# Performance work log

Hardware: AMD Instinct MI355X
Metric: run time of the kernel (lower is better)

## Reference

```python
import jax, jax.numpy as jnp
import numpy as np

K_DT = 7
GAMMA_DT = 0.1
EPS = 1e-6
B_DIST = 3.0

def _make_kernels():
    # CDT kernel: exp(-dist/gamma), 7x7x7
    k = K_DT
    g = np.mgrid[0:k, 0:k, 0:k] - np.floor(k / 2)
    dist = np.sqrt((g ** 2).sum(axis=0))
    cdt_k = np.exp(-dist / GAMMA_DT)[None, None].astype(np.float32)  # [1,1,7,7,7]
    # 27-point Laplacian
    lap = (1.0 / 26.0) * np.array(
        [[[2, 3, 2], [3, 6, 3], [2, 3, 2]],
         [[3, 6, 3], [6, -88, 6], [3, 6, 3]],
         [[2, 3, 2], [3, 6, 3], [2, 3, 2]]], dtype=np.float64)
    lap_k = lap[None, None].astype(np.float32)  # [1,1,3,3,3]
    # Scharr_2 Sobel-type gradient filters
    h1_p = np.array([[[1, 0, -1]]], dtype=np.float64)
    h1 = np.array([[[47, 162, 47]]], dtype=np.float64)
    h1 = h1 / h1.sum()
    h2 = h1.transpose(1, 2, 0); h2_p = h1_p.transpose(1, 2, 0)
    h3 = h1.transpose(2, 0, 1); h3_p = h1_p.transpose(2, 0, 1)
    G1 = np.kron(np.kron(h2, h3), h1_p)
    G2 = np.kron(np.kron(h3, h1), h2_p)
    G3 = np.kron(np.kron(h1, h2), h3_p)
    sob_k = np.stack([G1, G2, G3], axis=0)[:, None].astype(np.float32)  # [3,1,3,3,3]
    return jnp.asarray(cdt_k), jnp.asarray(lap_k), jnp.asarray(sob_k)

CDT_K, LAP_K, SOB_K = _make_kernels()

def conv3d(x, w, pad):
    return jax.lax.conv_general_dilated(
        x, w, window_strides=(1, 1, 1), padding=[(pad, pad)] * 3,
        dimension_numbers=('NCDHW', 'OIDHW', 'NCDHW'))

def binary(x, th, gamma):
    return jax.nn.sigmoid((x - th) * gamma)

def cdt(x):
    return -GAMMA_DT * jnp.log(conv3d(x, CDT_K, 3) + EPS)

def setup_inputs() -> dict:
    key = jax.random.key(0)
    k1, k2, k3 = jax.random.split(key, 3)
    B, C, D, H, W = 2, 1, 128, 192, 192
    x_in = jax.random.uniform(k1, (B, C, D, H, W), dtype=jnp.float32)
    y_out = jax.random.normal(k2, (B, C, D, H, W), dtype=jnp.float32)
    y_tg = jax.random.randint(k3, (B, C, D, H, W), 0, 2).astype(jnp.float32)
    w_smp = jnp.ones((1,), dtype=jnp.float32)
    gamma_ace = jnp.full((1,), 0.1, dtype=jnp.float32)
    return {"x_in": x_in, "y_out": y_out, "y_tg": y_tg, "w_smp": w_smp, "gamma_ace": gamma_ace}

def reference(x_in, y_out, y_tg, w_smp, gamma_ace):
    w_mean = jnp.mean(w_smp)
    # ---- CE_Loss (BCEWithLogits, pos_weight=1, stable form) ----
    ce_pt = jnp.clip(y_out, 0, None) - y_out * y_tg + jnp.log1p(jnp.exp(-jnp.abs(y_out)))
    ce_pm = jnp.mean(ce_pt, axis=(1, 2, 3))  # matches torch mean over dims (1,2,3)
    loss_ce = jnp.mean(w_smp * ce_pm) / w_mean
    # ---- Dice_Loss ----
    y_p = jax.nn.sigmoid(y_out)
    inter = jnp.sum(y_p * y_tg, axis=(1, 2, 3))
    card = jnp.sum(y_p + y_tg, axis=(1, 2, 3))
    d_loss = 1.0 - 2.0 * inter / (card + EPS)
    loss_dice = jnp.mean(w_smp * d_loss) / w_mean
    # ---- DT_Loss ----
    y_p_inv = 1.0 - y_p
    yb = binary(y_p, 0.5, 200.0)
    yb_inv = binary(y_p_inv, 0.5, 200.0)
    y_tg_inv = 1.0 - y_tg
    z = cdt(yb); z_tg = cdt(y_tg); z_inv = cdt(yb_inv); z_tg_inv = cdt(y_tg_inv)
    dl1 = jnp.mean(y_tg * z) / jnp.mean(y_tg + EPS)
    dl2 = jnp.mean(y_p * z_tg) / jnp.mean(y_p + EPS)
    dl3 = jnp.mean(y_tg_inv * z_inv) / jnp.mean(y_tg_inv + EPS)
    dl4 = jnp.mean(y_p_inv * z_tg_inv) / jnp.mean(y_p_inv + EPS)
    dt_pt = dl1 + dl2 + dl3 + dl4
    loss_dt = jnp.mean(w_smp * dt_pt) / w_mean
    # ---- ACE_Loss ----
    y = binary(y_p, 0.5, 200.0)
    y1 = binary(conv3d(y, LAP_K, 1), 0.5, 200.0)        # edge detector
    s = conv3d(y, SOB_K, 1)                              # [B,3,D,H,W]
    y2 = jnp.sqrt(jnp.sum(s * s, axis=1, keepdims=True) + EPS)
    y3 = jax.nn.relu(B_DIST - cdt(y))
    y4 = binary((B_DIST - y3) * binary(y3, 0.0, 200.0), 0.1, 200.0)
    l1 = jnp.mean(x_in * y, axis=(1, 2, 3, 4)) / jnp.mean(y + EPS, axis=(1, 2, 3, 4))
    l2 = jnp.mean(x_in * y4, axis=(1, 2, 3, 4)) / jnp.mean(y4 + EPS, axis=(1, 2, 3, 4))
    E1 = jnp.mean(y * (x_in - l1[:, None, None, None, None]) ** 2) / jnp.mean(y + EPS)
    E2 = jnp.mean(y4 * (x_in - l2[:, None, None, None, None]) ** 2) / jnp.mean(y4 + EPS)
    S = jnp.mean(y1 * y2) / jnp.mean(y1 + EPS)
    ace_pt = E1 + E2 + gamma_ace[0] * S
    loss_ace = jnp.mean(w_smp * ace_pt) / w_mean
    # ---- weighted sum ----
    w_ce, w_dt, w_ace, w_dice = 1.0, 0.1, 0.1, 1.0
    return w_ce * loss_ce + w_dice * loss_dice + w_dt * loss_dt + w_ace * loss_ace
```

## Files before the change

### kernel.cpp

```cpp
#include <hip/hip_runtime.h>
#include <hip/hip_bf16.h>

#define TH 8
#define TW 64
#define DC 16
#define PH (TH+2)
#define PW (TW+2)
#define PN (PH*PW)

#define DIM_D 128
#define DIM_H 192
#define DIM_W 192
#define NREP 16

#define LOG2E 1.4426950408889634f
#define LN2   0.6931471805599453f

__device__ __forceinline__ float ex2(float x){ return __builtin_amdgcn_exp2f(x); }
__device__ __forceinline__ float lg2(float x){ return __builtin_amdgcn_logf(x); }
__device__ __forceinline__ float rcpf_(float x){ return __builtin_amdgcn_rcpf(x); }
__device__ __forceinline__ float2 f2add(float2 a, float2 b){ return make_float2(a.x+b.x, a.y+b.y); }
__device__ __forceinline__ float2 f2fma(float s, float2 a, float2 b){
    return make_float2(fmaf(s,a.x,b.x), fmaf(s,a.y,b.y));
}

struct Pair { float2 u0[2], u1[2], u2[2]; float s1[2], s2[2]; };

__device__ __forceinline__ Pair calc_pair(const float2* __restrict__ sp, int ty, int tx)
{
    const float S30 = 47.f/256.f, S31 = 162.f/256.f;
    float2 c[3][4];
    #pragma unroll
    for (int r = 0; r < 3; ++r) {
        const float2* row = sp + (ty+r)*PW + 2*tx;
        float4 lo = *reinterpret_cast<const float4*>(row);
        float4 hi = *reinterpret_cast<const float4*>(row + 2);
        c[r][0] = make_float2(lo.x, lo.y); c[r][1] = make_float2(lo.z, lo.w);
        c[r][2] = make_float2(hi.x, hi.y); c[r][3] = make_float2(hi.z, hi.w);
    }
    float2 s[4], m[4]; float dj[4];
    #pragma unroll
    for (int j = 0; j < 4; ++j) {
        s[j] = f2add(c[0][j], c[2][j]);
        m[j] = c[1][j];
        dj[j] = c[0][j].x - c[2][j].x;
    }
    Pair P;
    float2 mm02 = f2add(m[0], m[2]), mm13 = f2add(m[1], m[3]);
    P.u0[0] = m[1];              P.u0[1] = m[2];
    P.u1[0] = f2add(s[1], mm02); P.u1[1] = f2add(s[2], mm13);
    P.u2[0] = f2add(s[0], s[2]); P.u2[1] = f2add(s[1], s[3]);
    P.s1[0] = S30*(s[0].x - s[2].x) + S31*(m[0].x - m[2].x);
    P.s1[1] = S30*(s[1].x - s[3].x) + S31*(m[1].x - m[3].x);
    P.s2[0] = S30*(dj[0] + dj[2]) + S31*dj[1];
    P.s2[1] = S30*(dj[1] + dj[3]) + S31*dj[2];
    return P;
}

__global__ __launch_bounds__(256) void lumen_main(
    const float* __restrict__ x_in, const float* __restrict__ y_out,
    const float* __restrict__ y_tg, double* __restrict__ gacc,
    float* __restrict__ dice_i, float* __restrict__ dice_c)
{
    __shared__ float2 ring[4][PN];

    const int tid = threadIdx.x;
    const int b  = blockIdx.z >> 3;
    const int d0 = (blockIdx.z & 7) * DC;
    const int h0 = blockIdx.y * TH;
    const int w0 = blockIdx.x * TW;
    const unsigned base = (unsigned)b * (unsigned)(DIM_D*DIM_H*DIM_W);
    const unsigned PL = DIM_H*DIM_W;
    const int rep = (blockIdx.x + gridDim.x*(blockIdx.y + gridDim.y*blockIdx.z)) & (NREP-1);

    const int l1v = tid + 256, l2v = tid + 512;
    const int dy0 = tid / PW, dx0 = tid - dy0*PW;
    const int dy1 = l1v / PW, dx1 = l1v - dy1*PW;
    const int dy2 = l2v / PW, dx2 = l2v - dy2*PW;
    const bool w2  = (l2v < PN);
    const int sgh0 = h0-1+dy0, sgw0 = w0-1+dx0;
    const int sgh1 = h0-1+dy1, sgw1 = w0-1+dx1;
    const int sgh2 = h0-1+dy2, sgw2 = w0-1+dx2;
    const bool ok0 = ((unsigned)sgh0 < (unsigned)DIM_H) && ((unsigned)sgw0 < (unsigned)DIM_W);
    const bool ok1 = ((unsigned)sgh1 < (unsigned)DIM_H) && ((unsigned)sgw1 < (unsigned)DIM_W);
    const bool ok2 = w2 && ((unsigned)sgh2 < (unsigned)DIM_H) && ((unsigned)sgw2 < (unsigned)DIM_W);
    const unsigned soff0 = ok0 ? (unsigned)(sgh0*DIM_W + sgw0) : 0u;
    const unsigned soff1 = ok1 ? (unsigned)(sgh1*DIM_W + sgw1) : 0u;
    const unsigned soff2 = ok2 ? (unsigned)(sgh2*DIM_W + sgw2) : 0u;

    float ld_yo0, ld_tg0, ld_yo1, ld_tg1, ld_yo2, ld_tg2;

    auto LOADP = [&](int p){
        if ((unsigned)p < (unsigned)DIM_D) {
            const unsigned pb = base + (unsigned)p*PL;
            float a0 = y_out[pb + soff0], c0 = y_tg[pb + soff0];
            float a1_ = y_out[pb + soff1], c1 = y_tg[pb + soff1];
            float a2_ = y_out[pb + soff2], c2 = y_tg[pb + soff2];
            ld_yo0 = ok0 ? a0 : -1e30f;  ld_tg0 = ok0 ? c0 : 0.f;
            ld_yo1 = ok1 ? a1_ : -1e30f; ld_tg1 = ok1 ? c1 : 0.f;
            ld_yo2 = ok2 ? a2_ : -1e30f; ld_tg2 = ok2 ? c2 : 0.f;
        } else {
            ld_yo0 = -1e30f; ld_tg0 = 0.f; ld_yo1 = -1e30f; ld_tg1 = 0.f;
            ld_yo2 = -1e30f; ld_tg2 = 0.f;
        }
    };
    auto WRITEP = [&](int slot){
        float yb0 = rcpf_(1.f + ex2(-50.f*LOG2E*ld_yo0));
        ring[slot][tid] = make_float2(yb0, ld_tg0);
        float yb1 = rcpf_(1.f + ex2(-50.f*LOG2E*ld_yo1));
        ring[slot][l1v] = make_float2(yb1, ld_tg1);
        if (w2) {
            float yb2 = rcpf_(1.f + ex2(-50.f*LOG2E*ld_yo2));
            ring[slot][l2v] = make_float2(yb2, ld_tg2);
        }
    };

    const int ty = tid >> 5, tx = tid & 31;
    const int gh = h0 + ty;
    const float2* xin2 = reinterpret_cast<const float2*>(x_in);
    const float2* yo2p = reinterpret_cast<const float2*>(y_out);
    const unsigned PL2 = PL >> 1;
    const unsigned cen2 = (base >> 1) + (unsigned)gh*(DIM_W/2) + (unsigned)(w0>>1) + (unsigned)tx;

    const float KC1 = 4.5399929762484854e-05f, KC2 = 7.2135410e-07f, KC3 = 3.0047e-08f;
    const float L0 = -88.f/26.f, L1 = 6.f/26.f, L2 = 3.f/26.f, L3 = 2.f/26.f;
    const float S30 = 47.f/256.f, S31 = 162.f/256.f;
    const float TFULL = 1.f + 6.f*KC1 + 12.f*KC2 + 8.f*KC3;
    const float Y4TH = 0.36787858f;

    LOADP(d0-1); WRITEP(3);
    LOADP(d0  ); WRITEP(0);
    LOADP(d0+1); WRITEP(1);
    LOADP(d0+2);
    __syncthreads();
    Pair PA = calc_pair(ring[3], ty, tx);
    Pair PB = calc_pair(ring[0], ty, tx);

    float a_ce=0, a_tz=0, a_pzt=0, a_itzi=0, a_ipzti=0, a_ytg=0;
    float a_y1y2=0, a_y1=0;
    float2 aE1 = make_float2(0.f,0.f);
    float2 aEx = make_float2(0.f,0.f);
    float2 aExx= make_float2(0.f,0.f);
    float dI0=0, dI1=0, dC0=0, dC1=0;

    #pragma unroll 2
    for (int i = 0; i < DC; ++i) {
        const int d = d0 + i;
        WRITEP((i+2)&3);
        __syncthreads();
        LOADP(d+3);
        float2 xc  = xin2[cen2 + (unsigned)d*PL2];
        float2 yoc = yo2p[cen2 + (unsigned)d*PL2];

        Pair PC = calc_pair(ring[(i+1)&3], ty, tx);

        #pragma unroll
        for (int v = 0; v < 2; ++v) {
            float2 q0 = f2add(PA.u0[v], PC.u0[v]);
            float2 q1 = f2add(PA.u1[v], PC.u1[v]);
            float2 q2 = f2add(PA.u2[v], PC.u2[v]);
            float2 acv = f2fma(KC3, q2,
                         f2fma(KC2, f2add(PB.u2[v], q1),
                         f2fma(KC1, f2add(PB.u1[v], q0), PB.u0[v])));
            float acx = acv.x, act = acv.y;
            float al  = L0*PB.u0[v].x + L1*(PB.u1[v].x + q0.x)
                      + L2*(PB.u2[v].x + q1.x) + L3*q2.x;
            float a1 = S30*(PA.s1[v] + PC.s1[v]) + S31*PB.s1[v];
            float a2 = S30*(PA.s2[v] + PC.s2[v]) + S31*PB.s2[v];
            float a3 = (S31*S31)*(PA.u0[v].x - PC.u0[v].x)
                     + (S30*S31)*(PA.u1[v].x - PC.u1[v].x)
                     + (S30*S30)*(PA.u2[v].x - PC.u2[v].x);

            float t   = PB.u0[v].y;
            float ybc = PB.u0[v].x;
            float x   = v ? xc.y  : xc.x;
            float yo  = v ? yoc.y : yoc.x;

            float ayo = fabsf(yo);
            float e1  = ex2(-LOG2E*ayo);
            float inv = rcpf_(1.f + e1);
            float yp  = (yo >= 0.f) ? inv : (1.f - inv);
            a_ce += fmaxf(yo, 0.f) - yo*t + LN2*lg2(1.f + e1);

            if (v) { dI1 += yp*t; dC1 += yp + t; }
            else   { dI0 += yp*t; dC0 += yp + t; }

            float l2a = lg2(acx + 1e-6f);
            float z   = -0.1f*LN2*l2a;
            a_tz    += t*z;
            a_pzt   += yp      * (-0.1f*LN2)*lg2(act + 1e-6f);
            a_itzi  += (1.f-t) * (-0.1f*LN2)*lg2((TFULL - acx) + 1e-6f);
            a_ipzti += (1.f-yp)* (-0.1f*LN2)*lg2((TFULL - act) + 1e-6f);
            a_ytg   += t;

            float y2 = __builtin_amdgcn_sqrtf(a1*a1 + a2*a2 + a3*a3 + 1e-6f);
            bool e1b = (al > 0.5f);
            a_y1y2 += e1b ? y2 : 0.f;
            a_y1   += e1b ? 1.f : 0.f;

            float y4 = (acx < Y4TH) ? 1.f : 0.f;
            float2 w24 = make_float2(ybc, y4);
            aE1  = f2add(aE1, w24);
            aEx  = f2fma(x,   w24, aEx);
            aExx = f2fma(x*x, w24, aExx);
        }

        PA = PB; PB = PC;
    }

    float a_yp = (dC0 + dC1) - a_ytg;

    dI0 += __shfl_xor(dI0, 32);  dI1 += __shfl_xor(dI1, 32);
    dC0 += __shfl_xor(dC0, 32);  dC1 += __shfl_xor(dC1, 32);

    float v[15] = {a_ce, a_tz, a_pzt, a_itzi, a_ipzti, a_yp, a_ytg, a_y1y2, a_y1,
                   aE1.x, aEx.x, aExx.x, aE1.y, aEx.y, aExx.y};
    #pragma unroll
    for (int k = 0; k < 15; ++k) {
        #pragma unroll
        for (int s = 32; s > 0; s >>= 1) v[k] += __shfl_xor(v[k], s);
    }

    __syncthreads();
    float* sl = (float*)ring;
    if (tid < 128) sl[tid] = 0.f;
    __syncthreads();

    int wid = tid >> 6, lane = tid & 63;
    if (lane < 32) {
        atomicAdd(&sl[2*lane],       dI0);
        atomicAdd(&sl[2*lane+1],     dI1);
        atomicAdd(&sl[64 + 2*lane],  dC0);
        atomicAdd(&sl[64 + 2*lane+1],dC1);
    }
    if (lane == 0) {
        #pragma unroll
        for (int k = 0; k < 15; ++k) sl[128 + wid*16 + k] = v[k];
    }
    __syncthreads();

    if (tid < 15) {
        float s = sl[128+tid] + sl[144+tid] + sl[160+tid] + sl[176+tid];
        int gidx = (tid < 9) ? tid : (9 + (tid - 9)*2 + b);
        atomicAdd(&gacc[rep*24 + gidx], (double)s);
    }
    if (tid < 64) {
        atomicAdd(&dice_i[b*DIM_W + w0 + tid], sl[tid]);
        atomicAdd(&dice_c[b*DIM_W + w0 + tid], sl[64 + tid]);
    }
}

__global__ __launch_bounds__(256) void lumen_final(
    const double* __restrict__ gacc,
    const float* __restrict__ dice_i, const float* __restrict__ dice_c,
    const float* __restrict__ gamma_ace, float* __restrict__ out)
{
    __shared__ float red[4];
    __shared__ double gs[24];
    int tid = threadIdx.x;
    if (tid < 24) {
        double sr = 0.0;
        for (int r = 0; r < NREP; ++r) sr += gacc[r*24 + tid];
        gs[tid] = sr;
    }
    float s = 0.f;
    for (int i = tid; i < 2*DIM_W; i += 256) {
        float I = dice_i[i], C = dice_c[i];
        s += 1.f - 2.f*I/(C + 1e-6f);
    }
    #pragma unroll
    for (int sh = 32; sh > 0; sh >>= 1) s += __shfl_xor(s, sh);
    if ((tid & 63) == 0) red[tid >> 6] = s;
    __syncthreads();
    if (tid == 0) {
        double dice_sum = (double)red[0] + red[1] + red[2] + red[3];
        double loss_dice = dice_sum / (2.0*DIM_W);
        const double Nb = (double)DIM_D * DIM_H * DIM_W;
        const double Nt = 2.0 * Nb;
        const double eps = 1e-6;
        double loss_ce = gs[0]/Nt;
        double dl1 = (gs[1]/Nt) / ((gs[6]/Nt) + eps);
        double dl2 = (gs[2]/Nt) / ((gs[5]/Nt) + eps);
        double dl3 = (gs[3]/Nt) / (((Nt - gs[6])/Nt) + eps);
        double dl4 = (gs[4]/Nt) / (((Nt - gs[5])/Nt) + eps);
        double loss_dt = dl1 + dl2 + dl3 + dl4;
        double E1n = 0.0, E2n = 0.0;
        for (int bb = 0; bb < 2; ++bb) {
            double S1 = gs[9+bb],  Sx = gs[11+bb], Sxx = gs[13+bb];
            double l1 = (Sx/Nb) / ((S1/Nb) + eps);
            E1n += Sxx - 2.0*l1*Sx + l1*l1*S1;
            double Q1 = gs[15+bb], Qx = gs[17+bb], Qxx = gs[19+bb];
            double l2 = (Qx/Nb) / ((Q1/Nb) + eps);
            E2n += Qxx - 2.0*l2*Qx + l2*l2*Q1;
        }
        double E1 = (E1n/Nt) / (((gs[9]+gs[10])/Nt) + eps);
        double E2 = (E2n/Nt) / (((gs[15]+gs[16])/Nt) + eps);
        double S  = (gs[7]/Nt) / ((gs[8]/Nt) + eps);
        double loss_ace = E1 + E2 + (double)gamma_ace[0]*S;
        out[0] = (float)(loss_ce + loss_dice + 0.1*loss_dt + 0.1*loss_ace);
    }
}

extern "C" void kernel_launch(void* const* d_in, const int* in_sizes, int n_in,
                              void* d_out, int out_size, void* d_ws, size_t ws_size,
                              hipStream_t stream) {
    const float* x_in  = (const float*)d_in[0];
    const float* y_out = (const float*)d_in[1];
    const float* y_tg  = (const float*)d_in[2];
    const float* gamma = (const float*)d_in[4];
    float* out = (float*)d_out;

    double* gacc  = (double*)d_ws;
    float* dice_i = (float*)((char*)d_ws + 4096);
    float* dice_c = (float*)((char*)d_ws + 6144);

    hipMemsetAsync(d_ws, 0, 8192, stream);

    dim3 grid(DIM_W/TW, DIM_H/TH, 2*(DIM_D/DC));
    lumen_main<<<grid, 256, 0, stream>>>(x_in, y_out, y_tg, gacc, dice_i, dice_c);
    lumen_final<<<1, 256, 0, stream>>>(gacc, dice_i, dice_c, gamma, out);
}
```

Baseline: 79.57 us.

## Software-pipeline LDS plane reads and center loads one slice ahead

```diff
diff --git a/kernel.cpp b/kernel.cpp
--- a/kernel.cpp
+++ b/kernel.cpp
@@ -24,26 +24,32 @@
     return make_float2(fmaf(s,a.x,b.x), fmaf(s,a.y,b.y));
 }
 
+struct Raw  { float2 c[3][4]; };
 struct Pair { float2 u0[2], u1[2], u2[2]; float s1[2], s2[2]; };
 
-__device__ __forceinline__ Pair calc_pair(const float2* __restrict__ sp, int ty, int tx)
+__device__ __forceinline__ Raw load_raw(const float2* __restrict__ sp, int ty, int tx)
 {
-    const float S30 = 47.f/256.f, S31 = 162.f/256.f;
-    float2 c[3][4];
+    Raw R;
     #pragma unroll
     for (int r = 0; r < 3; ++r) {
         const float2* row = sp + (ty+r)*PW + 2*tx;
         float4 lo = *reinterpret_cast<const float4*>(row);
         float4 hi = *reinterpret_cast<const float4*>(row + 2);
-        c[r][0] = make_float2(lo.x, lo.y); c[r][1] = make_float2(lo.z, lo.w);
-        c[r][2] = make_float2(hi.x, hi.y); c[r][3] = make_float2(hi.z, hi.w);
-    }
+        R.c[r][0] = make_float2(lo.x, lo.y); R.c[r][1] = make_float2(lo.z, lo.w);
+        R.c[r][2] = make_float2(hi.x, hi.y); R.c[r][3] = make_float2(hi.z, hi.w);
+    }
+    return R;
+}
+
+__device__ __forceinline__ Pair reduce_raw(const Raw& R)
+{
+    const float S30 = 47.f/256.f, S31 = 162.f/256.f;
     float2 s[4], m[4]; float dj[4];
     #pragma unroll
     for (int j = 0; j < 4; ++j) {
-        s[j] = f2add(c[0][j], c[2][j]);
-        m[j] = c[1][j];
-        dj[j] = c[0][j].x - c[2][j].x;
+        s[j] = f2add(R.c[0][j], R.c[2][j]);
+        m[j] = R.c[1][j];
+        dj[j] = R.c[0][j].x - R.c[2][j].x;
     }
     Pair P;
     float2 mm02 = f2add(m[0], m[2]), mm13 = f2add(m[1], m[3]);
@@ -132,9 +138,12 @@
     LOADP(d0  ); WRITEP(0);
     LOADP(d0+1); WRITEP(1);
     LOADP(d0+2);
-    __syncthreads();
-    Pair PA = calc_pair(ring[3], ty, tx);
-    Pair PB = calc_pair(ring[0], ty, tx);
+    float2 xc  = xin2[cen2 + (unsigned)d0*PL2];
+    float2 yoc = yo2p[cen2 + (unsigned)d0*PL2];
+    __syncthreads();
+    Pair PA = reduce_raw(load_raw(ring[3], ty, tx));
+    Pair PB = reduce_raw(load_raw(ring[0], ty, tx));
+    Pair PC = reduce_raw(load_raw(ring[1], ty, tx));
 
     float a_ce=0, a_tz=0, a_pzt=0, a_itzi=0, a_ipzti=0, a_ytg=0;
     float a_y1y2=0, a_y1=0;
@@ -148,11 +157,11 @@
         const int d = d0 + i;
         WRITEP((i+2)&3);
         __syncthreads();
-        LOADP(d+3);
-        float2 xc  = xin2[cen2 + (unsigned)d*PL2];
-        float2 yoc = yo2p[cen2 + (unsigned)d*PL2];
-
-        Pair PC = calc_pair(ring[(i+1)&3], ty, tx);
+        Raw RD = load_raw(ring[(i+2)&3], ty, tx);
+        if (i < DC-1) LOADP(d+3);
+        const int dn = min(d+1, DIM_D-1);
+        float2 xn  = xin2[cen2 + (unsigned)dn*PL2];
+        float2 yon = yo2p[cen2 + (unsigned)dn*PL2];
 
         #pragma unroll
         for (int v = 0; v < 2; ++v) {
@@ -205,7 +214,9 @@
             aExx = f2fma(x*x, w24, aExx);
         }
 
-        PA = PB; PB = PC;
+        Pair PD = reduce_raw(RD);
+        PA = PB; PB = PC; PC = PD;
+        xc = xn; yoc = yon;
     }
 
     float a_yp = (dC0 + dC1) - a_ytg;
```

After: 91.82 us. 1.15x slower.

## Store smoothed ring buffer as half2, halve depth chunk, prefetch center loads

Applied to the files above, without the earlier changes.

```diff
diff --git a/kernel.cpp b/kernel.cpp
--- a/kernel.cpp
+++ b/kernel.cpp
@@ -1,9 +1,10 @@
 #include <hip/hip_runtime.h>
 #include <hip/hip_bf16.h>
+#include <hip/hip_fp16.h>
 
 #define TH 8
 #define TW 64
-#define DC 16
+#define DC 8
 #define PH (TH+2)
 #define PW (TW+2)
 #define PN (PH*PW)
@@ -19,39 +20,37 @@
 __device__ __forceinline__ float ex2(float x){ return __builtin_amdgcn_exp2f(x); }
 __device__ __forceinline__ float lg2(float x){ return __builtin_amdgcn_logf(x); }
 __device__ __forceinline__ float rcpf_(float x){ return __builtin_amdgcn_rcpf(x); }
-__device__ __forceinline__ float2 f2add(float2 a, float2 b){ return make_float2(a.x+b.x, a.y+b.y); }
-__device__ __forceinline__ float2 f2fma(float s, float2 a, float2 b){
-    return make_float2(fmaf(s,a.x,b.x), fmaf(s,a.y,b.y));
-}
-
-struct Pair { float2 u0[2], u1[2], u2[2]; float s1[2], s2[2]; };
-
-__device__ __forceinline__ Pair calc_pair(const float2* __restrict__ sp, int ty, int tx)
+__device__ __forceinline__ __half2 bch2(unsigned u){ return __builtin_bit_cast(__half2, u); }
+
+struct PairH { __half2 u0[2], u1[2], u2[2]; float s1[2], s2[2]; };
+
+__device__ __forceinline__ PairH calc_pair(const __half2* __restrict__ sp, int ty, int tx)
 {
     const float S30 = 47.f/256.f, S31 = 162.f/256.f;
-    float2 c[3][4];
+    __half2 c[3][4];
     #pragma unroll
     for (int r = 0; r < 3; ++r) {
-        const float2* row = sp + (ty+r)*PW + 2*tx;
-        float4 lo = *reinterpret_cast<const float4*>(row);
-        float4 hi = *reinterpret_cast<const float4*>(row + 2);
-        c[r][0] = make_float2(lo.x, lo.y); c[r][1] = make_float2(lo.z, lo.w);
-        c[r][2] = make_float2(hi.x, hi.y); c[r][3] = make_float2(hi.z, hi.w);
-    }
-    float2 s[4], m[4]; float dj[4];
+        const __half2* row = sp + (ty+r)*PW + 2*tx;
+        uint2 lo = *reinterpret_cast<const uint2*>(row);
+        uint2 hi = *reinterpret_cast<const uint2*>(row + 2);
+        c[r][0]=bch2(lo.x); c[r][1]=bch2(lo.y); c[r][2]=bch2(hi.x); c[r][3]=bch2(hi.y);
+    }
+    __half2 s[4], m[4]; float dj[4];
     #pragma unroll
     for (int j = 0; j < 4; ++j) {
-        s[j] = f2add(c[0][j], c[2][j]);
+        s[j] = __hadd2(c[0][j], c[2][j]);
         m[j] = c[1][j];
-        dj[j] = c[0][j].x - c[2][j].x;
-    }
-    Pair P;
-    float2 mm02 = f2add(m[0], m[2]), mm13 = f2add(m[1], m[3]);
-    P.u0[0] = m[1];              P.u0[1] = m[2];
-    P.u1[0] = f2add(s[1], mm02); P.u1[1] = f2add(s[2], mm13);
-    P.u2[0] = f2add(s[0], s[2]); P.u2[1] = f2add(s[1], s[3]);
-    P.s1[0] = S30*(s[0].x - s[2].x) + S31*(m[0].x - m[2].x);
-    P.s1[1] = S30*(s[1].x - s[3].x) + S31*(m[1].x - m[3].x);
+        dj[j] = __low2float(__hsub2(c[0][j], c[2][j]));
+    }
+    PairH P;
+    __half2 mm02 = __hadd2(m[0], m[2]), mm13 = __hadd2(m[1], m[3]);
+    P.u0[0] = m[1];                 P.u0[1] = m[2];
+    P.u1[0] = __hadd2(s[1], mm02);  P.u1[1] = __hadd2(s[2], mm13);
+    P.u2[0] = __hadd2(s[0], s[2]);  P.u2[1] = __hadd2(s[1], s[3]);
+    float s0x=__low2float(s[0]), s1x=__low2float(s[1]), s2x=__low2float(s[2]), s3x=__low2float(s[3]);
+    float m0x=__low2float(m[0]), m1x=__low2float(m[1]), m2x=__low2float(m[2]), m3x=__low2float(m[3]);
+    P.s1[0] = S30*(s0x - s2x) + S31*(m0x - m2x);
+    P.s1[1] = S30*(s1x - s3x) + S31*(m1x - m3x);
     P.s2[0] = S30*(dj[0] + dj[2]) + S31*dj[1];
     P.s2[1] = S30*(dj[1] + dj[3]) + S31*dj[2];
     return P;
@@ -62,11 +61,11 @@
     const float* __restrict__ y_tg, double* __restrict__ gacc,
     float* __restrict__ dice_i, float* __restrict__ dice_c)
 {
-    __shared__ float2 ring[4][PN];
+    __shared__ __half2 ring[4][PN];
 
     const int tid = threadIdx.x;
-    const int b  = blockIdx.z >> 3;
-    const int d0 = (blockIdx.z & 7) * DC;
+    const int b  = blockIdx.z >> 4;
+    const int d0 = (blockIdx.z & 15) * DC;
     const int h0 = blockIdx.y * TH;
     const int w0 = blockIdx.x * TW;
     const unsigned base = (unsigned)b * (unsigned)(DIM_D*DIM_H*DIM_W);
@@ -106,12 +105,12 @@
     };
     auto WRITEP = [&](int slot){
         float yb0 = rcpf_(1.f + ex2(-50.f*LOG2E*ld_yo0));
-        ring[slot][tid] = make_float2(yb0, ld_tg0);
+        ring[slot][tid] = __floats2half2_rn(yb0, ld_tg0);
         float yb1 = rcpf_(1.f + ex2(-50.f*LOG2E*ld_yo1));
-        ring[slot][l1v] = make_float2(yb1, ld_tg1);
+        ring[slot][l1v] = __floats2half2_rn(yb1, ld_tg1);
         if (w2) {
             float yb2 = rcpf_(1.f + ex2(-50.f*LOG2E*ld_yo2));
-            ring[slot][l2v] = make_float2(yb2, ld_tg2);
+            ring[slot][l2v] = __floats2half2_rn(yb2, ld_tg2);
         }
     };
 
@@ -132,9 +131,11 @@
     LOADP(d0  ); WRITEP(0);
     LOADP(d0+1); WRITEP(1);
     LOADP(d0+2);
-    __syncthreads();
-    Pair PA = calc_pair(ring[3], ty, tx);
-    Pair PB = calc_pair(ring[0], ty, tx);
+    float2 xc  = xin2[cen2 + (unsigned)d0*PL2];
+    float2 yoc = yo2p[cen2 + (unsigned)d0*PL2];
+    __syncthreads();
+    PairH PA = calc_pair(ring[3], ty, tx);
+    PairH PB = calc_pair(ring[0], ty, tx);
 
     float a_ce=0, a_tz=0, a_pzt=0, a_itzi=0, a_ipzti=0, a_ytg=0;
     float a_y1y2=0, a_y1=0;
@@ -149,30 +150,34 @@
         WRITEP((i+2)&3);
         __syncthreads();
         LOADP(d+3);
-        float2 xc  = xin2[cen2 + (unsigned)d*PL2];
-        float2 yoc = yo2p[cen2 + (unsigned)d*PL2];
-
-        Pair PC = calc_pair(ring[(i+1)&3], ty, tx);
+        const int dn = min(d+1, DIM_D-1);
+        float2 xn  = xin2[cen2 + (unsigned)dn*PL2];
+        float2 yon = yo2p[cen2 + (unsigned)dn*PL2];
+
+        PairH PC = calc_pair(ring[(i+1)&3], ty, tx);
 
         #pragma unroll
         for (int v = 0; v < 2; ++v) {
-            float2 q0 = f2add(PA.u0[v], PC.u0[v]);
-            float2 q1 = f2add(PA.u1[v], PC.u1[v]);
-            float2 q2 = f2add(PA.u2[v], PC.u2[v]);
-            float2 acv = f2fma(KC3, q2,
-                         f2fma(KC2, f2add(PB.u2[v], q1),
-                         f2fma(KC1, f2add(PB.u1[v], q0), PB.u0[v])));
-            float acx = acv.x, act = acv.y;
-            float al  = L0*PB.u0[v].x + L1*(PB.u1[v].x + q0.x)
-                      + L2*(PB.u2[v].x + q1.x) + L3*q2.x;
+            __half2 q0 = __hadd2(PA.u0[v], PC.u0[v]);
+            __half2 q1 = __hadd2(PA.u1[v], PC.u1[v]);
+            __half2 q2 = __hadd2(PA.u2[v], PC.u2[v]);
+            __half2 n1 = __hadd2(PB.u1[v], q0);
+            __half2 n2 = __hadd2(PB.u2[v], q1);
+            float m0x = __low2float(PB.u0[v]), m0y = __high2float(PB.u0[v]);
+            float n1x = __low2float(n1), n1y = __high2float(n1);
+            float n2x = __low2float(n2), n2y = __high2float(n2);
+            float n3x = __low2float(q2), n3y = __high2float(q2);
+            float acx = fmaf(KC3,n3x, fmaf(KC2,n2x, fmaf(KC1,n1x, m0x)));
+            float act = fmaf(KC3,n3y, fmaf(KC2,n2y, fmaf(KC1,n1y, m0y)));
+            float al  = fmaf(L3,n3x, fmaf(L2,n2x, fmaf(L1,n1x, L0*m0x)));
             float a1 = S30*(PA.s1[v] + PC.s1[v]) + S31*PB.s1[v];
             float a2 = S30*(PA.s2[v] + PC.s2[v]) + S31*PB.s2[v];
-            float a3 = (S31*S31)*(PA.u0[v].x - PC.u0[v].x)
-                     + (S30*S31)*(PA.u1[v].x - PC.u1[v].x)
-                     + (S30*S30)*(PA.u2[v].x - PC.u2[v].x);
-
-            float t   = PB.u0[v].y;
-            float ybc = PB.u0[v].x;
+            float a3 = (S31*S31)*__low2float(__hsub2(PA.u0[v], PC.u0[v]))
+                     + (S30*S31)*__low2float(__hsub2(PA.u1[v], PC.u1[v]))
+                     + (S30*S30)*__low2float(__hsub2(PA.u2[v], PC.u2[v]));
+
+            float t   = m0y;
+            float ybc = m0x;
             float x   = v ? xc.y  : xc.x;
             float yo  = v ? yoc.y : yoc.x;
 
@@ -199,13 +204,13 @@
             a_y1   += e1b ? 1.f : 0.f;
 
             float y4 = (acx < Y4TH) ? 1.f : 0.f;
-            float2 w24 = make_float2(ybc, y4);
-            aE1  = f2add(aE1, w24);
-            aEx  = f2fma(x,   w24, aEx);
-            aExx = f2fma(x*x, w24, aExx);
+            aE1.x  += ybc;            aE1.y  += y4;
+            aEx.x   = fmaf(x,   ybc, aEx.x);   aEx.y   = fmaf(x,   y4, aEx.y);
+            aExx.x  = fmaf(x*x, ybc, aExx.x);  aExx.y  = fmaf(x*x, y4, aExx.y);
         }
 
         PA = PB; PB = PC;
+        xc = xn; yoc = yon;
     }
 
     float a_yp = (dC0 + dC1) - a_ytg;
```

Result: faster. 75.06 us (-5.7%).
